# Performance work log

Measured on AMD Instinct MI355X. Metric: run time of the kernel, lower is better.

## Reference

```python
import jax, jax.numpy as jnp
import numpy as np

# Constants matching the module's forward-time configuration
NUM_STAGES = 2
HIDDEN_LENGTH = (512, 1024)   # per-stage video token lengths; S = sum = 1536
ENC_LEN = 128                 # text/encoder token length per sample
B, H, D = 8, 16, 64           # batch (interleaved over stages), heads, head_dim
SEQLENS = (np.array([640, 480, 560, 400], np.int32),     # valid lens, stage 0 (Lc=640)
           np.array([1152, 864, 1008, 720], np.int32))   # valid lens, stage 1 (Lc=1152)


def _pack_indices(seqlens, lc):
    return np.concatenate([i * lc + np.arange(l) for i, l in enumerate(seqlens)]).astype(np.int32)


def setup_inputs() -> dict:
    key = jax.random.key(0)
    ks = jax.random.split(key, 6)
    S = sum(HIDDEN_LENGTH)
    inp = {
        'query':         jax.random.normal(ks[0], (B, S, H, D), jnp.float32),
        'key':           jax.random.normal(ks[1], (B, S, H, D), jnp.float32),
        'value':         jax.random.normal(ks[2], (B, S, H, D), jnp.float32),
        'encoder_query': jax.random.normal(ks[3], (B, ENC_LEN, H, D), jnp.float32),
        'encoder_key':   jax.random.normal(ks[4], (B, ENC_LEN, H, D), jnp.float32),
        'encoder_value': jax.random.normal(ks[5], (B, ENC_LEN, H, D), jnp.float32),
        'indices_0': jnp.asarray(_pack_indices(SEQLENS[0], ENC_LEN + HIDDEN_LENGTH[0])),
        'indices_1': jnp.asarray(_pack_indices(SEQLENS[1], ENC_LEN + HIDDEN_LENGTH[1])),
        'seqlens_0': jnp.asarray(SEQLENS[0]),
        'seqlens_1': jnp.asarray(SEQLENS[1]),
        'heads': 16,
        'scale': jnp.asarray(0.125, jnp.float32),  # 1/sqrt(D)
    }
    return inp


def reference(query, key, value, encoder_query, encoder_key, encoder_value,
              indices_0, indices_1, seqlens_0, seqlens_1, heads, scale):
    # Per stage: take the interleaved batch slice, prepend encoder tokens,
    # run non-causal varlen attention (padded + key-masked == flash_attn_varlen),
    # then gather the valid (packed) rows — faithful to index_first_axis packing.
    indices = (indices_0, indices_1)
    seqlens = (seqlens_0, seqlens_1)
    neg = jnp.finfo(query.dtype).min
    outs = []
    i_sum = 0
    for idx, L in enumerate(HIDDEN_LENGTH):
        q_s = jnp.concatenate([encoder_query[idx::NUM_STAGES], query[idx::NUM_STAGES, i_sum:i_sum + L]], axis=1)
        k_s = jnp.concatenate([encoder_key[idx::NUM_STAGES],   key[idx::NUM_STAGES,   i_sum:i_sum + L]], axis=1)
        v_s = jnp.concatenate([encoder_value[idx::NUM_STAGES], value[idx::NUM_STAGES, i_sum:i_sum + L]], axis=1)
        lc = q_s.shape[1]                                    # enc_len + L
        kmask = jnp.arange(lc)[None, :] < seqlens[idx][:, None]   # [b, lc] key validity
        scores = jnp.einsum('bqhd,bkhd->bhqk', q_s, k_s) * scale  # [b,h,lc,lc]
        scores = jnp.where(kmask[:, None, None, :], scores, neg)
        attn = jax.nn.softmax(scores, axis=-1)
        o = jnp.einsum('bhqk,bkhd->bqhd', attn, v_s)              # [b,lc,h,d]
        o_flat = o.reshape(-1, o.shape[2], o.shape[3])            # [(b*lc),h,d]
        outs.append(o_flat[indices[idx]])                          # pack valid rows
        i_sum += L
    return jnp.concatenate(outs, axis=0)  # [total_packed_tokens, H, D]
```

## Files before the change

### kernel.cpp

```cpp
#include <hip/hip_runtime.h>
#include <hip/hip_bf16.h>

typedef __attribute__((ext_vector_type(8))) __bf16 bf16x8;
typedef __attribute__((ext_vector_type(8))) short short8;
typedef __attribute__((ext_vector_type(4))) float f32x4;
typedef __attribute__((ext_vector_type(4))) unsigned int uint4v;
typedef __attribute__((ext_vector_type(2))) unsigned int uint2v;

#define KS 72
#define LOG2E 1.44269504088896340736f

__device__ __forceinline__ unsigned pack2bf(float lo, float hi) {
    unsigned a = __builtin_bit_cast(unsigned, lo) + 0x8000u;
    unsigned b = __builtin_bit_cast(unsigned, hi) + 0x8000u;
    return __builtin_amdgcn_perm(b, a, 0x07060302u);
}

__device__ __forceinline__ bf16x8 ldfrag(const short* p) {
    short8 s = *reinterpret_cast<const short8*>(p);
    return __builtin_bit_cast(bf16x8, s);
}

__global__ __launch_bounds__(512, 8) void vfa_kernel(
    const float* __restrict__ qv, const float* __restrict__ kv, const float* __restrict__ vv,
    const float* __restrict__ eq, const float* __restrict__ ek, const float* __restrict__ ev,
    const float* __restrict__ scale_p, float* __restrict__ out)
{
    constexpr int H = 16, Dh = 64, ENC = 128, SV = 1536;
    constexpr int SS_CUM[9] = {0,144,272,384,480,560,640,704,768};
    constexpr int SEQL[8] = {1152,1008,864,720,640,560,480,400};
    constexpr int QTN[8]  = {9,8,7,6,5,5,4,4};
    constexpr int OB[8]   = {2080,4096,3232,5104,0,1120,640,1680};
    constexpr int BB[8]   = {1,5,3,7,0,4,2,6};
    constexpr int ISUM[8] = {512,512,512,512,0,0,0,0};

    __shared__ __align__(16) short smem[2*64*KS];
    short* kbuf = smem;
    short* vbuf = smem + 64*KS;

    const int bid = blockIdx.x;
    int ss = 0;
    #pragma unroll
    for (int i = 1; i < 8; ++i) ss += (bid >= SS_CUM[i]) ? 1 : 0;
    const int seqlen   = SEQL[ss];
    const int nqt      = QTN[ss];
    const int b        = BB[ss];
    const int isum     = ISUM[ss];
    const int out_base = OB[ss];
    const int local    = bid - SS_CUM[ss];
    const int head     = local / nqt;
    const int qt       = local - head * nqt;

    const int tid  = threadIdx.x;
    const int wave = tid >> 6;
    const int lane = tid & 63;
    const int quad = lane >> 4;
    const int l15  = lane & 15;

    const float qmul = scale_p[0] * LOG2E;

    const int qrow = qt*128 + wave*16 + l15;
    const float* qrp;
    if (qrow < ENC) qrp = eq + ((b*ENC + qrow)*H + head)*Dh;
    else            qrp = qv + (((b*SV + isum) + (qrow - ENC))*H + head)*Dh;
    bf16x8 qfrag[2];
    #pragma unroll
    for (int f = 0; f < 2; ++f) {
        const float* p = qrp + f*32 + quad*8;
        f32x4 a = *reinterpret_cast<const f32x4*>(p);
        f32x4 c = *reinterpret_cast<const f32x4*>(p + 4);
        uint4v u;
        u[0] = pack2bf(a[0]*qmul, a[1]*qmul);
        u[1] = pack2bf(a[2]*qmul, a[3]*qmul);
        u[2] = pack2bf(c[0]*qmul, c[1]*qmul);
        u[3] = pack2bf(c[2]*qmul, c[3]*qmul);
        qfrag[f] = __builtin_bit_cast(bf16x8, u);
    }

    f32x4 acc[4];
    #pragma unroll
    for (int dt = 0; dt < 4; ++dt) acc[dt] = {0.f,0.f,0.f,0.f};
    float m_s = -INFINITY, l_s = 0.f;

    const int t2  = tid & 255;
    const int klk = t2 >> 2;
    const int kd  = (t2 & 3) * 16;
    const int vk0 = (t2 & 15) * 4;
    const int vd0 = (t2 >> 4) * 4;

    const int nkt = (seqlen + 63) >> 6;
    const int src_base = l15 + ((quad & 1) << 5);

    for (int kt = 0; kt < nkt; ++kt) {
        if (kt) __syncthreads();
        if (tid < 256) {
            const int kr = kt*64 + klk;
            const float* krow;
            if (kr < ENC) krow = ek + ((b*ENC + kr)*H + head)*Dh;
            else          krow = kv + (((b*SV + isum) + (kr - ENC))*H + head)*Dh;
            f32x4 kf0 = *reinterpret_cast<const f32x4*>(krow + kd);
            f32x4 kf1 = *reinterpret_cast<const f32x4*>(krow + kd + 4);
            f32x4 kf2 = *reinterpret_cast<const f32x4*>(krow + kd + 8);
            f32x4 kf3 = *reinterpret_cast<const f32x4*>(krow + kd + 12);
            uint4v kp;
            kp[0] = pack2bf(kf0[0], kf0[1]);
            kp[1] = pack2bf(kf0[2], kf0[3]);
            kp[2] = pack2bf(kf1[0], kf1[1]);
            kp[3] = pack2bf(kf1[2], kf1[3]);
            *reinterpret_cast<uint4v*>(&kbuf[klk*KS + kd]) = kp;
            kp[0] = pack2bf(kf2[0], kf2[1]);
            kp[1] = pack2bf(kf2[2], kf2[3]);
            kp[2] = pack2bf(kf3[0], kf3[1]);
            kp[3] = pack2bf(kf3[2], kf3[3]);
            *reinterpret_cast<uint4v*>(&kbuf[klk*KS + kd + 8]) = kp;
        } else {
            f32x4 vf[4];
            #pragma unroll
            for (int i = 0; i < 4; ++i) {
                const int kr = kt*64 + vk0 + i;
                const float* vrow;
                if (kr < ENC) vrow = ev + ((b*ENC + kr)*H + head)*Dh;
                else          vrow = vv + (((b*SV + isum) + (kr - ENC))*H + head)*Dh;
                vf[i] = *reinterpret_cast<const f32x4*>(vrow + vd0);
            }
            #pragma unroll
            for (int j = 0; j < 4; ++j) {
                uint2v w;
                w[0] = pack2bf(vf[0][j], vf[1][j]);
                w[1] = pack2bf(vf[2][j], vf[3][j]);
                *reinterpret_cast<uint2v*>(&vbuf[(vd0 + j)*KS + vk0]) = w;
            }
        }
        __syncthreads();

        const int rem  = seqlen - kt*64;
        const int nsub = (rem >= 64) ? 4 : (rem >> 4);

        float s[4][4];
        #pragma unroll
        for (int sub = 0; sub < 4; ++sub) {
            if (sub < nsub) {
                const short* kr0 = &kbuf[(sub*16 + l15)*KS + quad*8];
                f32x4 sv = {0.f,0.f,0.f,0.f};
                sv = __builtin_amdgcn_mfma_f32_16x16x32_bf16(ldfrag(kr0),      qfrag[0], sv, 0,0,0);
                sv = __builtin_amdgcn_mfma_f32_16x16x32_bf16(ldfrag(kr0 + 32), qfrag[1], sv, 0,0,0);
                #pragma unroll
                for (int r = 0; r < 4; ++r) s[sub][r] = sv[r];
            } else {
                #pragma unroll
                for (int r = 0; r < 4; ++r) s[sub][r] = -INFINITY;
            }
        }

        float mx = s[0][0];
        #pragma unroll
        for (int sub = 0; sub < 4; ++sub)
            #pragma unroll
            for (int r = 0; r < 4; ++r) mx = fmaxf(mx, s[sub][r]);
        mx = fmaxf(mx, __shfl_xor(mx, 16, 64));
        mx = fmaxf(mx, __shfl_xor(mx, 32, 64));
        const float mn = fmaxf(m_s, mx);
        const float alpha = __builtin_amdgcn_exp2f(m_s - mn);
        m_s = mn;
        #pragma unroll
        for (int dt = 0; dt < 4; ++dt)
            #pragma unroll
            for (int r = 0; r < 4; ++r) acc[dt][r] *= alpha;

        float rs = 0.f;
        unsigned pk[4][2];
        #pragma unroll
        for (int sub = 0; sub < 4; ++sub) {
            float p0 = __builtin_amdgcn_exp2f(s[sub][0] - mn);
            float p1 = __builtin_amdgcn_exp2f(s[sub][1] - mn);
            float p2 = __builtin_amdgcn_exp2f(s[sub][2] - mn);
            float p3 = __builtin_amdgcn_exp2f(s[sub][3] - mn);
            rs += (p0 + p1) + (p2 + p3);
            pk[sub][0] = pack2bf(p0, p1);
            pk[sub][1] = pack2bf(p2, p3);
        }
        rs += __shfl_xor(rs, 16, 64);
        rs += __shfl_xor(rs, 32, 64);
        l_s = l_s * alpha + rs;

        #pragma unroll
        for (int kstep = 0; kstep < 2; ++kstep) {
            if (kstep == 0 || nsub > 2) {
                uint4v pf;
                #pragma unroll
                for (int p = 0; p < 4; ++p) {
                    const int sl = src_base + ((p >> 1) << 4);
                    int va = __shfl((int)pk[kstep*2 + 0][p & 1], sl, 64);
                    int vb = __shfl((int)pk[kstep*2 + 1][p & 1], sl, 64);
                    pf[p] = (quad & 2) ? (unsigned)vb : (unsigned)va;
                }
                bf16x8 pfr = __builtin_bit_cast(bf16x8, pf);
                #pragma unroll
                for (int dt = 0; dt < 4; ++dt) {
                    bf16x8 vfr = ldfrag(&vbuf[(dt*16 + l15)*KS + kstep*32 + quad*8]);
                    acc[dt] = __builtin_amdgcn_mfma_f32_16x16x32_bf16(vfr, pfr, acc[dt], 0,0,0);
                }
            }
        }
    }

    __syncthreads();
    float* tbuf = reinterpret_cast<float*>(smem);
    const float inv = 1.0f / l_s;
    const int rowl = tid >> 3;
    const int colb = (tid & 7) * 8;
    #pragma unroll
    for (int p = 0; p < 2; ++p) {
        if (p) __syncthreads();
        if ((wave >> 2) == p) {
            #pragma unroll
            for (int dt = 0; dt < 4; ++dt) {
                f32x4 t = acc[dt] * inv;
                *reinterpret_cast<f32x4*>(&tbuf[((wave & 3)*16 + l15)*68 + dt*16 + quad*4]) = t;
            }
        }
        __syncthreads();
        const int grow = qt*128 + p*64 + rowl;
        if (grow < seqlen) {
            float* orow = out + (size_t)(out_base + grow)*(H*Dh) + head*Dh + colb;
            const float* trow = tbuf + rowl*68 + colb;
            *reinterpret_cast<float4*>(orow)     = *reinterpret_cast<const float4*>(trow);
            *reinterpret_cast<float4*>(orow + 4) = *reinterpret_cast<const float4*>(trow + 4);
        }
    }
}

extern "C" void kernel_launch(void* const* d_in, const int* in_sizes, int n_in,
                              void* d_out, int out_size, void* d_ws, size_t ws_size,
                              hipStream_t stream) {
    const float* q     = (const float*)d_in[0];
    const float* k     = (const float*)d_in[1];
    const float* v     = (const float*)d_in[2];
    const float* eq    = (const float*)d_in[3];
    const float* ek    = (const float*)d_in[4];
    const float* ev    = (const float*)d_in[5];
    const float* scale = (const float*)d_in[11];
    float* out = (float*)d_out;

    vfa_kernel<<<dim3(768), dim3(512), 0, stream>>>(q, k, v, eq, ek, ev, scale, out);
}
```

Before: 210.9 us.

## Double-buffer K/V tiles in LDS and prefetch next tile into registers

The K/V tile staging now uses two LDS buffers. Global loads for the next tile are issued into registers before the current tile's compute starts, so fetch latency overlaps the MFMA and softmax work, and one of the two barriers per iteration is removed. The cost is doubled shared memory (about 36KB per block) plus extra live registers for prefetching, which is why the launch-bounds occupancy hint is lowered from 8 to 6. The barrier is issued manually after an lgkmcnt wait and relies on the alternating buffers to avoid write-after-read races.

```diff
diff --git a/kernel.cpp b/kernel.cpp
--- a/kernel.cpp
+++ b/kernel.cpp
@@ -21,7 +21,7 @@
     return __builtin_bit_cast(bf16x8, s);
 }
 
-__global__ __launch_bounds__(512, 8) void vfa_kernel(
+__global__ __launch_bounds__(512, 6) void vfa_kernel(
     const float* __restrict__ qv, const float* __restrict__ kv, const float* __restrict__ vv,
     const float* __restrict__ eq, const float* __restrict__ ek, const float* __restrict__ ev,
     const float* __restrict__ scale_p, float* __restrict__ out)
@@ -34,9 +34,7 @@
     constexpr int BB[8]   = {1,5,3,7,0,4,2,6};
     constexpr int ISUM[8] = {512,512,512,512,0,0,0,0};
 
-    __shared__ __align__(16) short smem[2*64*KS];
-    short* kbuf = smem;
-    short* vbuf = smem + 64*KS;
+    __shared__ __align__(16) short smem[4*64*KS];
 
     const int bid = blockIdx.x;
     int ss = 0;
@@ -87,51 +85,73 @@
     const int kd  = (t2 & 3) * 16;
     const int vk0 = (t2 & 15) * 4;
     const int vd0 = (t2 >> 4) * 4;
+    const bool krole = (tid < 256);
 
     const int nkt = (seqlen + 63) >> 6;
     const int src_base = l15 + ((quad & 1) << 5);
 
-    for (int kt = 0; kt < nkt; ++kt) {
-        if (kt) __syncthreads();
-        if (tid < 256) {
-            const int kr = kt*64 + klk;
+    f32x4 ld0, ld1, ld2, ld3;
+
+    auto issue_loads = [&](int kt_) {
+        if (krole) {
+            const int kr = kt_*64 + klk;
             const float* krow;
             if (kr < ENC) krow = ek + ((b*ENC + kr)*H + head)*Dh;
             else          krow = kv + (((b*SV + isum) + (kr - ENC))*H + head)*Dh;
-            f32x4 kf0 = *reinterpret_cast<const f32x4*>(krow + kd);
-            f32x4 kf1 = *reinterpret_cast<const f32x4*>(krow + kd + 4);
-            f32x4 kf2 = *reinterpret_cast<const f32x4*>(krow + kd + 8);
-            f32x4 kf3 = *reinterpret_cast<const f32x4*>(krow + kd + 12);
-            uint4v kp;
-            kp[0] = pack2bf(kf0[0], kf0[1]);
-            kp[1] = pack2bf(kf0[2], kf0[3]);
-            kp[2] = pack2bf(kf1[0], kf1[1]);
-            kp[3] = pack2bf(kf1[2], kf1[3]);
-            *reinterpret_cast<uint4v*>(&kbuf[klk*KS + kd]) = kp;
-            kp[0] = pack2bf(kf2[0], kf2[1]);
-            kp[1] = pack2bf(kf2[2], kf2[3]);
-            kp[2] = pack2bf(kf3[0], kf3[1]);
-            kp[3] = pack2bf(kf3[2], kf3[3]);
-            *reinterpret_cast<uint4v*>(&kbuf[klk*KS + kd + 8]) = kp;
+            ld0 = *reinterpret_cast<const f32x4*>(krow + kd);
+            ld1 = *reinterpret_cast<const f32x4*>(krow + kd + 4);
+            ld2 = *reinterpret_cast<const f32x4*>(krow + kd + 8);
+            ld3 = *reinterpret_cast<const f32x4*>(krow + kd + 12);
         } else {
-            f32x4 vf[4];
             #pragma unroll
             for (int i = 0; i < 4; ++i) {
-                const int kr = kt*64 + vk0 + i;
+                const int kr = kt_*64 + vk0 + i;
                 const float* vrow;
                 if (kr < ENC) vrow = ev + ((b*ENC + kr)*H + head)*Dh;
                 else          vrow = vv + (((b*SV + isum) + (kr - ENC))*H + head)*Dh;
-                vf[i] = *reinterpret_cast<const f32x4*>(vrow + vd0);
-            }
+                f32x4 t = *reinterpret_cast<const f32x4*>(vrow + vd0);
+                if (i == 0) ld0 = t; else if (i == 1) ld1 = t;
+                else if (i == 2) ld2 = t; else ld3 = t;
+            }
+        }
+    };
+
+    auto write_tile = [&](short* kb, short* vb) {
+        if (krole) {
+            uint4v kp;
+            kp[0] = pack2bf(ld0[0], ld0[1]);
+            kp[1] = pack2bf(ld0[2], ld0[3]);
+            kp[2] = pack2bf(ld1[0], ld1[1]);
+            kp[3] = pack2bf(ld1[2], ld1[3]);
+            *reinterpret_cast<uint4v*>(&kb[klk*KS + kd]) = kp;
+            kp[0] = pack2bf(ld2[0], ld2[1]);
+            kp[1] = pack2bf(ld2[2], ld2[3]);
+            kp[2] = pack2bf(ld3[0], ld3[1]);
+            kp[3] = pack2bf(ld3[2], ld3[3]);
+            *reinterpret_cast<uint4v*>(&kb[klk*KS + kd + 8]) = kp;
+        } else {
             #pragma unroll
             for (int j = 0; j < 4; ++j) {
                 uint2v w;
-                w[0] = pack2bf(vf[0][j], vf[1][j]);
-                w[1] = pack2bf(vf[2][j], vf[3][j]);
-                *reinterpret_cast<uint2v*>(&vbuf[(vd0 + j)*KS + vk0]) = w;
-            }
-        }
-        __syncthreads();
+                w[0] = pack2bf(ld0[j], ld1[j]);
+                w[1] = pack2bf(ld2[j], ld3[j]);
+                *reinterpret_cast<uint2v*>(&vb[(vd0 + j)*KS + vk0]) = w;
+            }
+        }
+    };
+
+    issue_loads(0);
+
+    for (int kt = 0; kt < nkt; ++kt) {
+        short* kb = smem + (kt & 1) * (2*64*KS);
+        short* vb = kb + 64*KS;
+
+        write_tile(kb, vb);
+        if (kt + 1 < nkt) issue_loads(kt + 1);
+
+        asm volatile("s_waitcnt lgkmcnt(0)" ::: "memory");
+        __builtin_amdgcn_s_barrier();
+        __builtin_amdgcn_sched_barrier(0);
 
         const int rem  = seqlen - kt*64;
         const int nsub = (rem >= 64) ? 4 : (rem >> 4);
@@ -140,7 +160,7 @@
         #pragma unroll
         for (int sub = 0; sub < 4; ++sub) {
             if (sub < nsub) {
-                const short* kr0 = &kbuf[(sub*16 + l15)*KS + quad*8];
+                const short* kr0 = &kb[(sub*16 + l15)*KS + quad*8];
                 f32x4 sv = {0.f,0.f,0.f,0.f};
                 sv = __builtin_amdgcn_mfma_f32_16x16x32_bf16(ldfrag(kr0),      qfrag[0], sv, 0,0,0);
                 sv = __builtin_amdgcn_mfma_f32_16x16x32_bf16(ldfrag(kr0 + 32), qfrag[1], sv, 0,0,0);
@@ -191,13 +211,13 @@
                 for (int p = 0; p < 4; ++p) {
                     const int sl = src_base + ((p >> 1) << 4);
                     int va = __shfl((int)pk[kstep*2 + 0][p & 1], sl, 64);
-                    int vb = __shfl((int)pk[kstep*2 + 1][p & 1], sl, 64);
-                    pf[p] = (quad & 2) ? (unsigned)vb : (unsigned)va;
+                    int vb2 = __shfl((int)pk[kstep*2 + 1][p & 1], sl, 64);
+                    pf[p] = (quad & 2) ? (unsigned)vb2 : (unsigned)va;
                 }
                 bf16x8 pfr = __builtin_bit_cast(bf16x8, pf);
                 #pragma unroll
                 for (int dt = 0; dt < 4; ++dt) {
-                    bf16x8 vfr = ldfrag(&vbuf[(dt*16 + l15)*KS + kstep*32 + quad*8]);
+                    bf16x8 vfr = ldfrag(&vb[(dt*16 + l15)*KS + kstep*32 + quad*8]);
                     acc[dt] = __builtin_amdgcn_mfma_f32_16x16x32_bf16(vfr, pfr, acc[dt], 0,0,0);
                 }
             }
```

New measurement: 206.9 us. No clear change (-1.9%).
